# Kernel optimization log

Measured on AMD Instinct MI355X. Metric: run time of the kernel, lower is better.

Reference implementation:

```python
import jax, jax.numpy as jnp
import numpy as np

N, E, F_IN, G = 50000, 800000, 128, 256
LAYERS = [(128, 4, 64), (256, 4, 64), (256, 1, 64)]  # (fan_in, heads, per-head dim)


def setup_inputs() -> dict:
    key = jax.random.key(0)
    ks = iter(jax.random.split(key, 64))
    nrm = lambda shp, s=1.0: jax.random.normal(next(ks), shp, jnp.float32) * s
    d = {}
    d["x"] = nrm((N, F_IN))
    d["edge_index"] = jax.random.randint(next(ks), (2, E), 0, N, dtype=jnp.int32)
    d["batch"] = jnp.sort(jax.random.randint(next(ks), (N,), 0, G, dtype=jnp.int32))
    for i, (fin, h, c) in enumerate(LAYERS):
        d[f"w{i}"] = nrm((fin, h * c), 1.0 / np.sqrt(fin))
        d[f"asrc{i}"] = nrm((h, c), 0.1)
        d[f"adst{i}"] = nrm((h, c), 0.1)
        d[f"b{i}"] = nrm((h * c,), 0.1)
        d[f"g{i}"] = 1.0 + nrm((h * c,), 0.1)
        d[f"be{i}"] = nrm((h * c,), 0.1)
        d[f"m{i}"] = nrm((h * c,), 0.1)
        d[f"v{i}"] = jnp.abs(nrm((h * c,), 0.1)) + 1.0
    d["fc1w"] = nrm((192, 64), 1.0 / np.sqrt(192)); d["fc1b"] = nrm((64,), 0.1)
    d["fc2w"] = nrm((64, 32), 1.0 / np.sqrt(64));   d["fc2b"] = nrm((32,), 0.1)
    d["fc3w"] = nrm((32, 1), 1.0 / np.sqrt(32));    d["fc3b"] = nrm((1,), 0.1)
    return d


def _gat_layer(x, w, a_s, a_d, b, src, dst, n, heads):
    c = w.shape[1] // heads
    h = (x @ w).reshape(n, heads, c)                      # [N,H,C]
    al_s = jnp.sum(h * a_s[None], axis=-1)                # [N,H]
    al_d = jnp.sum(h * a_d[None], axis=-1)                # [N,H]
    e = jax.nn.leaky_relu(al_s[src] + al_d[dst], 0.2)     # [E',H]
    emax = jax.ops.segment_max(e, dst, num_segments=n)
    emax = jnp.where(jnp.isfinite(emax), emax, 0.0)
    ee = jnp.exp(e - emax[dst])
    den = jax.ops.segment_sum(ee, dst, num_segments=n)
    alpha = ee / (den[dst] + 1e-16)                       # edge softmax per dst node
    out = jax.ops.segment_sum(h[src] * alpha[..., None], dst, num_segments=n)
    return out.reshape(n, heads * c) + b


def _bn(x, g, be, m, v):
    return (x - m) * jax.lax.rsqrt(v + 1e-5) * g + be


def reference(x, edge_index, batch,
              w0, asrc0, adst0, b0, g0, be0, m0, v0,
              w1, asrc1, adst1, b1, g1, be1, m1, v1,
              w2, asrc2, adst2, b2, g2, be2, m2, v2,
              fc1w, fc1b, fc2w, fc2b, fc3w, fc3b):
    n = x.shape[0]
    loop = jnp.arange(n, dtype=edge_index.dtype)          # add_self_loops (PyG default)
    src = jnp.concatenate([edge_index[0], loop])
    dst = jnp.concatenate([edge_index[1], loop])
    layers = [(w0, asrc0, adst0, b0, g0, be0, m0, v0, 4),
              (w1, asrc1, adst1, b1, g1, be1, m1, v1, 4),
              (w2, asrc2, adst2, b2, g2, be2, m2, v2, 1)]
    for (w, a_s, a_d, b, g, be, m, v, heads) in layers:
        x = _gat_layer(x, w, a_s, a_d, b, src, dst, n, heads)
        x = jax.nn.elu(_bn(x, g, be, m, v))
    # multi-pool readout over graphs
    xsum = jax.ops.segment_sum(x, batch, num_segments=G)
    cnt = jax.ops.segment_sum(jnp.ones((n, 1), x.dtype), batch, num_segments=G)
    xmean = xsum / jnp.maximum(cnt, 1.0)
    xmax = jax.ops.segment_max(x, batch, num_segments=G)
    xmax = jnp.where(jnp.isfinite(xmax), xmax, 0.0)
    h = jnp.concatenate([xmean, xmax, xsum], axis=1)      # [G, 192]
    h = jax.nn.relu(h @ fc1w + fc1b)
    h = jax.nn.relu(h @ fc2w + fc2b)
    return h @ fc3w + fc3b                                # [G, 1]
```

## Files before the change

kernel.cpp:

```cpp
#include <hip/hip_runtime.h>
#include <hip/hip_fp16.h>

typedef unsigned short ushort_t;
typedef unsigned int uint_t;
typedef __attribute__((ext_vector_type(8))) _Float16 half8;
typedef __attribute__((ext_vector_type(4))) float f32x4;

#define NN 50000
#define NE 800000
#define NGR 256
#define MAXDEG 64

typedef __attribute__((address_space(3))) unsigned int as3_u32;
typedef const __attribute__((address_space(1))) unsigned int as1_u32c;
__device__ __forceinline__ void gld16(const ushort_t* g, void* lds_base) {
    __builtin_amdgcn_global_load_lds((as1_u32c*)g, (as3_u32*)lds_base, 16, 0, 0);
}

__global__ void k_prep(const float* __restrict__ x0, __half* __restrict__ xf,
                       const float* __restrict__ W0, const float* __restrict__ W1,
                       const float* __restrict__ W2, __half* __restrict__ th,
                       int* __restrict__ colv, int* __restrict__ deg) {
    int i = blockIdx.x * 256 + threadIdx.x;
    if (i < 1600000) {
        float4 v = ((const float4*)x0)[i];
        __half2 a = __floats2half2_rn(v.x, v.y);
        __half2 b = __floats2half2_rn(v.z, v.w);
        *(__half2*)(xf + i * 4) = a;
        *(__half2*)(xf + i * 4 + 2) = b;
    } else if (i < 1600000 + 114688) {
        int w = i - 1600000;
        const float* W; int K, NC, idx, base;
        if (w < 32768)      { W = W0; K = 128; NC = 256; idx = w;         base = 0; }
        else if (w < 98304) { W = W1; K = 256; NC = 256; idx = w - 32768; base = 32768; }
        else                { W = W2; K = 256; NC = 64;  idx = w - 98304; base = 98304; }
        int k = idx / NC, n = idx % NC;
        th[base + n * K + k] = __float2half(W[idx]);
    } else if (i < 1600000 + 114688 + NN) {
        int n = i - 1714688;
        colv[n << 6] = n;
        deg[n] = 1;
    }
}

template<int KD, int BN>
__device__ __forceinline__ void gemm_body(int bx, int by,
    const __half* __restrict__ Ax, const __half* __restrict__ Bth,
    __half* __restrict__ Hout, const float* __restrict__ a_s,
    const float* __restrict__ a_d, float* __restrict__ als,
    float* __restrict__ ald, int H, int M, int NC) {
    constexpr int BM = 128, BK = 32;
    __shared__ ushort_t sA[BM * BK];
    __shared__ ushort_t sB[BN * BK];
    const int tid = threadIdx.x;
    const int m0 = bx * BM;
    const int n0 = by * BN;
    const int wv = tid >> 6, ln = tid & 63;
    const int lrow = ln & 15, lq = ln >> 4;
    constexpr int RT = (BN == 128) ? 4 : 2;
    int wm, wn;
    if constexpr (BN == 128) { wm = (wv >> 1) * 64; wn = (wv & 1) * 64; }
    else                     { wm = wv * 32;        wn = 0; }
    const int roff = ln >> 2;
    const int coff = (ln & 3) * 8;

    f32x4 acc[RT][4] = {};

    for (int k0 = 0; k0 < KD; k0 += BK) {
        #pragma unroll
        for (int ch = 0; ch < 2; ++ch) {
            int rb = wv * 32 + ch * 16;
            size_t ga = (size_t)(m0 + rb + roff) * KD + k0 + coff;
            gld16((const ushort_t*)Ax + ga, &sA[rb * BK]);
        }
        if constexpr (BN == 128) {
            #pragma unroll
            for (int ch = 0; ch < 2; ++ch) {
                int rb = wv * 32 + ch * 16;
                size_t gb = (size_t)(n0 + rb + roff) * KD + k0 + coff;
                gld16((const ushort_t*)Bth + gb, &sB[rb * BK]);
            }
        } else {
            int rb = wv * 16;
            size_t gb = (size_t)(n0 + rb + roff) * KD + k0 + coff;
            gld16((const ushort_t*)Bth + gb, &sB[rb * BK]);
        }
        __syncthreads();
        half8 af[RT], bf[4];
        #pragma unroll
        for (int r = 0; r < RT; ++r)
            af[r] = *(const half8*)&sA[(wm + r * 16 + lrow) * BK + lq * 8];
        #pragma unroll
        for (int c = 0; c < 4; ++c)
            bf[c] = *(const half8*)&sB[(wn + c * 16 + lrow) * BK + lq * 8];
        #pragma unroll
        for (int r = 0; r < RT; ++r)
            #pragma unroll
            for (int c = 0; c < 4; ++c)
                acc[r][c] = __builtin_amdgcn_mfma_f32_16x16x32_f16(af[r], bf[c], acc[r][c], 0, 0, 0);
        __syncthreads();
    }
    #pragma unroll
    for (int r = 0; r < RT; ++r) {
        #pragma unroll
        for (int c = 0; c < 4; ++c) {
            int colg = n0 + wn + c * 16 + lrow;
            #pragma unroll
            for (int j = 0; j < 4; ++j) {
                int row = m0 + wm + r * 16 + lq * 4 + j;
                if (row < M) Hout[(size_t)row * NC + colg] = __float2half(acc[r][c][j]);
            }
        }
    }
    int hh = (n0 + wn) >> 6;
    float asv[4], adv[4];
    #pragma unroll
    for (int c = 0; c < 4; ++c) {
        int cg = (n0 + wn + c * 16 + lrow) & 63;
        asv[c] = a_s[hh * 64 + cg];
        adv[c] = a_d[hh * 64 + cg];
    }
    #pragma unroll
    for (int r = 0; r < RT; ++r) {
        #pragma unroll
        for (int j = 0; j < 4; ++j) {
            float ts = 0.f, td = 0.f;
            #pragma unroll
            for (int c = 0; c < 4; ++c) {
                float v = acc[r][c][j];
                ts += v * asv[c];
                td += v * adv[c];
            }
            #pragma unroll
            for (int m = 1; m < 16; m <<= 1) {
                ts += __shfl_xor(ts, m);
                td += __shfl_xor(td, m);
            }
            int row = m0 + wm + r * 16 + lq * 4 + j;
            if (lrow == 0 && row < M) {
                als[row * H + hh] = ts;
                ald[row * H + hh] = td;
            }
        }
    }
}

template<int KD, int BN>
__global__ __launch_bounds__(256)
void k_mgemm(const __half* __restrict__ Ax, const __half* __restrict__ Bth,
             __half* __restrict__ Hout,
             const float* __restrict__ a_s, const float* __restrict__ a_d,
             float* __restrict__ als, float* __restrict__ ald,
             int H, int M, int NC) {
    gemm_body<KD, BN>(blockIdx.x, blockIdx.y, Ax, Bth, Hout, a_s, a_d, als, ald, H, M, NC);
}

__global__ __launch_bounds__(256)
void k_gf(const __half* __restrict__ Ax, const __half* __restrict__ Bth,
          __half* __restrict__ Hout,
          const float* __restrict__ a_s, const float* __restrict__ a_d,
          float* __restrict__ als, float* __restrict__ ald, int M,
          const int* __restrict__ esrc, const int* __restrict__ edst,
          int* __restrict__ deg, int* __restrict__ colv) {
    constexpr int FILLB = ((NE + 4095) / 4096) * 8;
    if (blockIdx.x >= FILLB) {
        int g = blockIdx.x - FILLB;
        gemm_body<128, 128>(g >> 1, g & 1, Ax, Bth, Hout,
                            a_s, a_d, als, ald, 4, M, 256);
    } else {
        int r = blockIdx.x & 7;
        int c = blockIdx.x >> 3;
        int base = c * 4096 + (int)threadIdx.x * 4;
        int4 dv[4], sv[4];
        #pragma unroll
        for (int u = 0; u < 4; ++u) {
            int b = base + u * 1024;
            bool ok = b < NE;
            int bb = ok ? b : 0;
            dv[u] = *(const int4*)(edst + bb);
            sv[u] = *(const int4*)(esrc + bb);
            if (!ok) { dv[u].x = -1; dv[u].y = -1; dv[u].z = -1; dv[u].w = -1; }
        }
        const int lo = r * 6250;
        #pragma unroll
        for (int u = 0; u < 4; ++u) {
            const int* dp = (const int*)&dv[u];
            const int* sp = (const int*)&sv[u];
            #pragma unroll
            for (int j = 0; j < 4; ++j) {
                int d = dp[j];
                if ((unsigned)(d - lo) < 6250u) {
                    int pos = atomicAdd(&deg[d], 1);
                    if (pos < MAXDEG) colv[(d << 6) + pos] = sp[j];
                }
            }
        }
    }
}

__global__ __launch_bounds__(256)
void k_fagg4s(const __half* __restrict__ h, const float* __restrict__ als,
              const float* __restrict__ ald, const int* __restrict__ deg,
              const int* __restrict__ colv,
              const float* __restrict__ bias, const float* __restrict__ gam,
              const float* __restrict__ bet, const float* __restrict__ mu,
              const float* __restrict__ var,
              __half* __restrict__ xo, int M) {
    __shared__ uint_t wraw[4][64];
    int wv = threadIdx.x >> 6;
    int half = blockIdx.x & 1;
    int node = (blockIdx.x >> 1) * 4 + wv;
    if (node >= M) return;
    int l = threadIdx.x & 63;
    int dg = deg[node];
    int rs = node << 6;

    float2 ad = *(const float2*)(ald + (size_t)node * 4 + half * 2);
    bool vld = l < dg;
    int s = colv[vld ? rs + l : rs];
    int cv = s;
    float2 av = *(const float2*)((const char*)als + ((size_t)(uint_t)s << 4) + half * 8);
    float e0 = av.x + ad.x; e0 = e0 > 0.f ? e0 : 0.2f * e0; e0 = vld ? __expf(e0) : 0.f;
    float e1 = av.y + ad.y; e1 = e1 > 0.f ? e1 : 0.2f * e1; e1 = vld ? __expf(e1) : 0.f;
    float d0 = e0, d1 = e1;
    __half2 p = __floats2half2_rn(e0, e1);
    wraw[wv][l] = *(uint_t*)&p;
    #pragma unroll
    for (int off = 1; off < 64; off <<= 1) {
        d0 += __shfl_xor(d0, off); d1 += __shfl_xor(d1, off);
    }

    float a0 = 0.f, a1 = 0.f;
    const uint_t shB = (uint_t)((l & 32) >> 1);
    const uint_t loffB = (uint_t)(half * 256 + l * 4);
    int nrem = dg;
    #pragma unroll
    for (int grp = 0; grp < 3; ++grp) {
        int g0 = grp * 24;
        if (g0 < nrem) {
            uint_t hu[3][8];
            #pragma unroll
            for (int bb = 0; bb < 3; ++bb) {
                if (g0 + bb * 8 < nrem) {
                    #pragma unroll
                    for (int u = 0; u < 8; ++u) {
                        int sv = __builtin_amdgcn_readlane(cv, g0 + bb * 8 + u);
                        const char* hp = (const char*)h + ((size_t)(uint_t)sv << 9);
                        hu[bb][u] = *(const uint_t*)(hp + loffB);
                    }
                }
            }
            #pragma unroll
            for (int bb = 0; bb < 3; ++bb) {
                if (g0 + bb * 8 < nrem) {
                    #pragma unroll
                    for (int u = 0; u < 8; ++u) {
                        int j = g0 + bb * 8 + u;
                        uint_t w = wraw[wv][j];
                        uint_t afv = w >> shB;
                        asm("v_fma_mix_f32 %0, %1, %2, %0 op_sel:[0,0,0] op_sel_hi:[1,1,0]"
                            : "+v"(a0) : "v"(afv), "v"(hu[bb][u]));
                        asm("v_fma_mix_f32 %0, %1, %2, %0 op_sel:[0,1,0] op_sel_hi:[1,1,0]"
                            : "+v"(a1) : "v"(afv), "v"(hu[bb][u]));
                    }
                }
            }
        }
    }

    float den = (l & 32) ? d1 : d0;
    float inv = 1.f / (den + 1e-16f);
    int chg = half * 128 + l * 2;
    float2 bi = *(const float2*)(bias + chg);
    float2 ga = *(const float2*)(gam + chg);
    float2 be = *(const float2*)(bet + chg);
    float2 m2 = *(const float2*)(mu + chg);
    float2 v2 = *(const float2*)(var + chg);
    float o0 = a0 * inv + bi.x;
    float o1 = a1 * inv + bi.y;
    float bn0 = (o0 - m2.x) * rsqrtf(v2.x + 1e-5f) * ga.x + be.x;
    float bn1 = (o1 - m2.y) * rsqrtf(v2.y + 1e-5f) * ga.y + be.y;
    float f0 = bn0 > 0.f ? bn0 : (__expf(bn0) - 1.f);
    float f1 = bn1 > 0.f ? bn1 : (__expf(bn1) - 1.f);
    __half2 pk = __floats2half2_rn(f0, f1);
    *(uint_t*)&xo[(size_t)node * 256 + chg] = *(uint_t*)&pk;
}

__global__ __launch_bounds__(256)
void k_fagg1(const __half* __restrict__ h, const float* __restrict__ als,
             const float* __restrict__ ald, const int* __restrict__ deg,
             const int* __restrict__ colv,
             const float* __restrict__ bias, const float* __restrict__ gam,
             const float* __restrict__ bet, const float* __restrict__ mu,
             const float* __restrict__ var,
             float* __restrict__ xf, int M) {
    __shared__ uint_t wraw[4][64];
    int node = blockIdx.x * 4 + (threadIdx.x >> 6);
    if (node >= M) return;
    int wv = (threadIdx.x >> 6) & 3;
    int l = threadIdx.x & 63;
    int dg = deg[node];
    int rs = node << 6;

    float ad = ald[node];
    bool vld = l < dg;
    int s = colv[vld ? rs + l : rs];
    int cv = s;
    float e = als[s] + ad; e = e > 0.f ? e : 0.2f * e; e = vld ? __expf(e) : 0.f;
    float d0 = e;
    wraw[wv][l] = __float_as_uint(e);
    #pragma unroll
    for (int off = 1; off < 64; off <<= 1) d0 += __shfl_xor(d0, off);

    float a0 = 0.f;
    int nrem = dg;
    #pragma unroll
    for (int grp = 0; grp < 3; ++grp) {
        int g0 = grp * 24;
        if (g0 < nrem) {
            uint_t hu[3][8];
            #pragma unroll
            for (int bb = 0; bb < 3; ++bb) {
                if (g0 + bb * 8 < nrem) {
                    #pragma unroll
                    for (int u = 0; u < 8; ++u) {
                        int sv = __builtin_amdgcn_readlane(cv, g0 + bb * 8 + u);
                        const ushort_t* hp = (const ushort_t*)h + ((size_t)(uint_t)sv << 6);
                        hu[bb][u] = (uint_t)hp[l];
                    }
                }
            }
            #pragma unroll
            for (int bb = 0; bb < 3; ++bb) {
                if (g0 + bb * 8 < nrem) {
                    #pragma unroll
                    for (int u = 0; u < 8; ++u) {
                        int j = g0 + bb * 8 + u;
                        uint_t wfv = wraw[wv][j];
                        asm("v_fma_mix_f32 %0, %1, %2, %0 op_sel:[0,0,0] op_sel_hi:[0,1,0]"
                            : "+v"(a0) : "v"(wfv), "v"(hu[bb][u]));
                    }
                }
            }
        }
    }

    float inv = 1.f / (d0 + 1e-16f);
    float o = a0 * inv + bias[l];
    float bn = (o - mu[l]) * rsqrtf(var[l] + 1e-5f) * gam[l] + bet[l];
    float fo = bn > 0.f ? bn : (__expf(bn) - 1.f);
    xf[(size_t)node * 64 + l] = fo;
}

__global__ __launch_bounds__(512)
void k_poolfc(const float* __restrict__ x, const int* __restrict__ batch,
              const float* __restrict__ fc1w, const float* __restrict__ fc1b,
              const float* __restrict__ fc2w, const float* __restrict__ fc2b,
              const float* __restrict__ fc3w, const float* __restrict__ fc3b,
              float* __restrict__ out, int M) {
    __shared__ float ssum[8][64];
    __shared__ float smax[8][64];
    __shared__ float hb[192];
    __shared__ float h1[64];
    __shared__ float h2[32];
    int g = blockIdx.x, t = threadIdx.x;
    int d = t & 63, sub = t >> 6;
    int lo = 0, hi = M;
    while (lo < hi) { int mid = (lo + hi) >> 1; if (batch[mid] < g) lo = mid + 1; else hi = mid; }
    int s = lo;
    lo = 0; hi = M;
    while (lo < hi) { int mid = (lo + hi) >> 1; if (batch[mid] < g + 1) lo = mid + 1; else hi = mid; }
    int e = lo;
    float sum = 0.f, mx = -3.0e38f;
    for (int n = s + sub; n < e; n += 8) {
        float v = x[(size_t)n * 64 + d];
        sum += v; mx = fmaxf(mx, v);
    }
    ssum[sub][d] = sum; smax[sub][d] = mx;
    __syncthreads();
    if (t < 64) {
        float sm = 0.f, m2 = -3.0e38f;
        #pragma unroll
        for (int k = 0; k < 8; ++k) { sm += ssum[k][t]; m2 = fmaxf(m2, smax[k][t]); }
        int cnt = e - s;
        hb[t] = sm / (float)(cnt > 1 ? cnt : 1);
        hb[64 + t] = (cnt == 0) ? 0.f : m2;
        hb[128 + t] = sm;
    }
    __syncthreads();
    if (t < 64) {
        float s1 = fc1b[t];
        for (int k = 0; k < 192; ++k) s1 += hb[k] * fc1w[k * 64 + t];
        h1[t] = fmaxf(s1, 0.f);
    }
    __syncthreads();
    if (t < 32) {
        float s2 = fc2b[t];
        for (int k = 0; k < 64; ++k) s2 += h1[k] * fc2w[k * 32 + t];
        h2[t] = fmaxf(s2, 0.f);
    }
    __syncthreads();
    if (t == 0) {
        float s3 = fc3b[0];
        for (int k = 0; k < 32; ++k) s3 += h2[k] * fc3w[k];
        out[g] = s3;
    }
}

extern "C" void kernel_launch(void* const* d_in, const int* in_sizes, int n_in,
                              void* d_out, int out_size, void* d_ws, size_t ws_size,
                              hipStream_t stream) {
    const float* x0     = (const float*)d_in[0];
    const int* ei       = (const int*)d_in[1];
    const int* batch    = (const int*)d_in[2];
    const float* W[3]   = {(const float*)d_in[3],  (const float*)d_in[11], (const float*)d_in[19]};
    const float* AS[3]  = {(const float*)d_in[4],  (const float*)d_in[12], (const float*)d_in[20]};
    const float* AD[3]  = {(const float*)d_in[5],  (const float*)d_in[13], (const float*)d_in[21]};
    const float* BI[3]  = {(const float*)d_in[6],  (const float*)d_in[14], (const float*)d_in[22]};
    const float* GA[3]  = {(const float*)d_in[7],  (const float*)d_in[15], (const float*)d_in[23]};
    const float* BE[3]  = {(const float*)d_in[8],  (const float*)d_in[16], (const float*)d_in[24]};
    const float* MU[3]  = {(const float*)d_in[9],  (const float*)d_in[17], (const float*)d_in[25]};
    const float* VA[3]  = {(const float*)d_in[10], (const float*)d_in[18], (const float*)d_in[26]};
    const float* fc1w = (const float*)d_in[27];
    const float* fc1b = (const float*)d_in[28];
    const float* fc2w = (const float*)d_in[29];
    const float* fc2b = (const float*)d_in[30];
    const float* fc3w = (const float*)d_in[31];
    const float* fc3b = (const float*)d_in[32];

    char* ws = (char*)d_ws;
    int*   colv   = (int*)  (ws);
    int*   deg    = (int*)  (ws + 12800000);
    float* als    = (float*)(ws + 13000192);
    float* ald    = (float*)(ws + 13800192);
    __half* wTh   = (__half*)(ws + 14600192);
    __half* h_buf = (__half*)(ws + 14829568);
    __half* xf16  = (__half*)(ws + 40429568);
    float* xpool  = (float*)(ws + 66054144);

    const int* esrc = ei;
    const int* edst = ei + NE;

    k_prep<<<(1600000 + 114688 + NN + 255) / 256, 256, 0, stream>>>(x0, xf16, W[0], W[1], W[2],
                                                                    wTh, colv, deg);

    const int GB = (NN + 127) / 128;
    const int FILLB = ((NE + 4095) / 4096) * 8;
    int nwb = (NN + 3) / 4;
    int nsb = nwb * 2;

    k_gf<<<FILLB + 782, 256, 0, stream>>>(xf16, wTh, h_buf, AS[0], AD[0], als, ald, NN,
                                          esrc, edst, deg, colv);
    k_fagg4s<<<nsb, 256, 0, stream>>>(h_buf, als, ald, deg, colv,
                                      BI[0], GA[0], BE[0], MU[0], VA[0], xf16, NN);
    k_mgemm<256, 128><<<dim3(GB, 2), 256, 0, stream>>>(xf16, wTh + 32768, h_buf,
                                                       AS[1], AD[1], als, ald, 4, NN, 256);
    k_fagg4s<<<nsb, 256, 0, stream>>>(h_buf, als, ald, deg, colv,
                                      BI[1], GA[1], BE[1], MU[1], VA[1], xf16, NN);
    k_mgemm<256, 64><<<dim3(GB, 1), 256, 0, stream>>>(xf16, wTh + 98304, h_buf,
                                                      AS[2], AD[2], als, ald, 1, NN, 64);
    k_fagg1<<<nwb, 256, 0, stream>>>(h_buf, als, ald, deg, colv,
                                     BI[2], GA[2], BE[2], MU[2], VA[2], xpool, NN);

    k_poolfc<<<NGR, 512, 0, stream>>>(xpool, batch, fc1w, fc1b, fc2w, fc2b, fc3w, fc3b,
                                      (float*)d_out, NN);
    (void)in_sizes; (void)n_in; (void)out_size; (void)ws_size;
}
```

Measured before the change: 384.4 us.

## Store adjacency source indices as 16-bit and split fill kernel from layer-0 GEMM

Changes the padded adjacency array colv from int32 to uint16, halving its footprint and the bytes written during the fill and read by the three aggregation kernels. The fused fill+GEMM kernel is split back into a separate fill kernel followed by the standard layer-0 GEMM launch. Node ids fit in 16 bits only because N=50000, which limits generality. Un-fusing drops the overlap between the atomic fill and the GEMM and adds one launch.

```diff
diff --git a/kernel.cpp b/kernel.cpp
--- a/kernel.cpp
+++ b/kernel.cpp
@@ -20,7 +20,7 @@
 __global__ void k_prep(const float* __restrict__ x0, __half* __restrict__ xf,
                        const float* __restrict__ W0, const float* __restrict__ W1,
                        const float* __restrict__ W2, __half* __restrict__ th,
-                       int* __restrict__ colv, int* __restrict__ deg) {
+                       ushort_t* __restrict__ colv, int* __restrict__ deg) {
     int i = blockIdx.x * 256 + threadIdx.x;
     if (i < 1600000) {
         float4 v = ((const float4*)x0)[i];
@@ -38,8 +38,40 @@
         th[base + n * K + k] = __float2half(W[idx]);
     } else if (i < 1600000 + 114688 + NN) {
         int n = i - 1714688;
-        colv[n << 6] = n;
+        colv[n << 6] = (ushort_t)n;
         deg[n] = 1;
+    }
+}
+
+__global__ __launch_bounds__(256)
+void k_fill(const int* __restrict__ esrc, const int* __restrict__ edst,
+            int* __restrict__ deg, ushort_t* __restrict__ colv) {
+    int r = blockIdx.x & 7;
+    int c = blockIdx.x >> 3;
+    int base = c * 4096 + (int)threadIdx.x * 4;
+    int4 dv[4], sv[4];
+    #pragma unroll
+    for (int u = 0; u < 4; ++u) {
+        int b = base + u * 1024;
+        bool ok = b < NE;
+        int bb = ok ? b : 0;
+        dv[u] = *(const int4*)(edst + bb);
+        sv[u] = *(const int4*)(esrc + bb);
+        if (!ok) { dv[u].x = -1; dv[u].y = -1; dv[u].z = -1; dv[u].w = -1; }
+    }
+    const int lo = r * 6250;
+    #pragma unroll
+    for (int u = 0; u < 4; ++u) {
+        const int* dp = (const int*)&dv[u];
+        const int* sp = (const int*)&sv[u];
+        #pragma unroll
+        for (int j = 0; j < 4; ++j) {
+            int d = dp[j];
+            if ((unsigned)(d - lo) < 6250u) {
+                int pos = atomicAdd(&deg[d], 1);
+                if (pos < MAXDEG) colv[(d << 6) + pos] = (ushort_t)sp[j];
+            }
+        }
     }
 }
 
@@ -156,52 +188,9 @@
 }
 
 __global__ __launch_bounds__(256)
-void k_gf(const __half* __restrict__ Ax, const __half* __restrict__ Bth,
-          __half* __restrict__ Hout,
-          const float* __restrict__ a_s, const float* __restrict__ a_d,
-          float* __restrict__ als, float* __restrict__ ald, int M,
-          const int* __restrict__ esrc, const int* __restrict__ edst,
-          int* __restrict__ deg, int* __restrict__ colv) {
-    constexpr int FILLB = ((NE + 4095) / 4096) * 8;
-    if (blockIdx.x >= FILLB) {
-        int g = blockIdx.x - FILLB;
-        gemm_body<128, 128>(g >> 1, g & 1, Ax, Bth, Hout,
-                            a_s, a_d, als, ald, 4, M, 256);
-    } else {
-        int r = blockIdx.x & 7;
-        int c = blockIdx.x >> 3;
-        int base = c * 4096 + (int)threadIdx.x * 4;
-        int4 dv[4], sv[4];
-        #pragma unroll
-        for (int u = 0; u < 4; ++u) {
-            int b = base + u * 1024;
-            bool ok = b < NE;
-            int bb = ok ? b : 0;
-            dv[u] = *(const int4*)(edst + bb);
-            sv[u] = *(const int4*)(esrc + bb);
-            if (!ok) { dv[u].x = -1; dv[u].y = -1; dv[u].z = -1; dv[u].w = -1; }
-        }
-        const int lo = r * 6250;
-        #pragma unroll
-        for (int u = 0; u < 4; ++u) {
-            const int* dp = (const int*)&dv[u];
-            const int* sp = (const int*)&sv[u];
-            #pragma unroll
-            for (int j = 0; j < 4; ++j) {
-                int d = dp[j];
-                if ((unsigned)(d - lo) < 6250u) {
-                    int pos = atomicAdd(&deg[d], 1);
-                    if (pos < MAXDEG) colv[(d << 6) + pos] = sp[j];
-                }
-            }
-        }
-    }
-}
-
-__global__ __launch_bounds__(256)
 void k_fagg4s(const __half* __restrict__ h, const float* __restrict__ als,
               const float* __restrict__ ald, const int* __restrict__ deg,
-              const int* __restrict__ colv,
+              const ushort_t* __restrict__ colv,
               const float* __restrict__ bias, const float* __restrict__ gam,
               const float* __restrict__ bet, const float* __restrict__ mu,
               const float* __restrict__ var,
@@ -217,7 +206,7 @@
 
     float2 ad = *(const float2*)(ald + (size_t)node * 4 + half * 2);
     bool vld = l < dg;
-    int s = colv[vld ? rs + l : rs];
+    int s = (int)colv[vld ? rs + l : rs];
     int cv = s;
     float2 av = *(const float2*)((const char*)als + ((size_t)(uint_t)s << 4) + half * 8);
     float e0 = av.x + ad.x; e0 = e0 > 0.f ? e0 : 0.2f * e0; e0 = vld ? __expf(e0) : 0.f;
@@ -289,7 +278,7 @@
 __global__ __launch_bounds__(256)
 void k_fagg1(const __half* __restrict__ h, const float* __restrict__ als,
              const float* __restrict__ ald, const int* __restrict__ deg,
-             const int* __restrict__ colv,
+             const ushort_t* __restrict__ colv,
              const float* __restrict__ bias, const float* __restrict__ gam,
              const float* __restrict__ bet, const float* __restrict__ mu,
              const float* __restrict__ var,
@@ -304,7 +293,7 @@
 
     float ad = ald[node];
     bool vld = l < dg;
-    int s = colv[vld ? rs + l : rs];
+    int s = (int)colv[vld ? rs + l : rs];
     int cv = s;
     float e = als[s] + ad; e = e > 0.f ? e : 0.2f * e; e = vld ? __expf(e) : 0.f;
     float d0 = e;
@@ -429,14 +418,14 @@
     const float* fc3b = (const float*)d_in[32];
 
     char* ws = (char*)d_ws;
-    int*   colv   = (int*)  (ws);
-    int*   deg    = (int*)  (ws + 12800000);
-    float* als    = (float*)(ws + 13000192);
-    float* ald    = (float*)(ws + 13800192);
-    __half* wTh   = (__half*)(ws + 14600192);
-    __half* h_buf = (__half*)(ws + 14829568);
-    __half* xf16  = (__half*)(ws + 40429568);
-    float* xpool  = (float*)(ws + 66054144);
+    ushort_t* colv = (ushort_t*)(ws);
+    int*   deg    = (int*)  (ws + 6400000);
+    float* als    = (float*)(ws + 6600192);
+    float* ald    = (float*)(ws + 7400192);
+    __half* wTh   = (__half*)(ws + 8200192);
+    __half* h_buf = (__half*)(ws + 8429568);
+    __half* xf16  = (__half*)(ws + 34029568);
+    float* xpool  = (float*)(ws + 59654144);
 
     const int* esrc = ei;
     const int* edst = ei + NE;
@@ -449,8 +438,9 @@
     int nwb = (NN + 3) / 4;
     int nsb = nwb * 2;
 
-    k_gf<<<FILLB + 782, 256, 0, stream>>>(xf16, wTh, h_buf, AS[0], AD[0], als, ald, NN,
-                                          esrc, edst, deg, colv);
+    k_fill<<<FILLB, 256, 0, stream>>>(esrc, edst, deg, colv);
+    k_mgemm<128, 128><<<dim3(GB, 2), 256, 0, stream>>>(xf16, wTh, h_buf,
+                                                       AS[0], AD[0], als, ald, 4, NN, 256);
     k_fagg4s<<<nsb, 256, 0, stream>>>(h_buf, als, ald, deg, colv,
                                       BI[0], GA[0], BE[0], MU[0], VA[0], xf16, NN);
     k_mgemm<256, 128><<<dim3(GB, 2), 256, 0, stream>>>(xf16, wTh + 32768, h_buf,
```

After: 398.2 us. 3.6% more time.
